# Kernel optimization log

Measured on AMD Instinct MI355X. Metric: run time of the kernel, lower is better.

Reference implementation:

```python
import jax, jax.numpy as jnp
import numpy as np

N_NODES = 100000
N_EDGES = 1600000
D_IN = 64
HID = 64
N_GRAPHS = 64
NEG_SLOPE = 0.2


def _glorot(k, shape):
    s = (6.0 / (shape[-2] + shape[-1])) ** 0.5
    return jax.random.uniform(k, shape, jnp.float32, -s, s)


def setup_inputs() -> dict:
    key = jax.random.key(0)
    ks = jax.random.split(key, 12)
    x = jax.random.normal(ks[0], (N_NODES, D_IN), jnp.float32)
    edge_index = jax.random.randint(ks[1], (2, N_EDGES), 0, N_NODES, dtype=jnp.int32)
    edge_attr = jax.random.normal(ks[2], (N_EDGES,), jnp.float32)
    batch = jnp.sort(jax.random.randint(ks[3], (N_NODES,), 0, N_GRAPHS, dtype=jnp.int32))
    inp = {"x": x, "edge_index": edge_index, "edge_attr": edge_attr, "batch": batch}
    dims = [(D_IN, HID), (HID, HID), (HID, HID)]
    for i, (din, dout) in enumerate(dims):
        inp[f"W{i}"] = _glorot(ks[4 + i], (din, dout))
        # att param is [1, heads=1, 2*out + nb_edge_feats=1] -> flatten to [2*out+1]
        inp[f"att{i}"] = _glorot(ks[7 + i], (1, 2 * dout + 1)).reshape(-1)
        inp[f"b{i}"] = jnp.zeros((dout,), jnp.float32)
    inp["Wf"] = _glorot(ks[10], (HID, 1))
    inp["bf"] = jnp.zeros((1,), jnp.float32)
    return inp


def _gat_layer(h, src, dst, e, valid, W, att, b, n):
    # MyGATConv (heads=1, concat=True): linear, per-edge attention logits,
    # leaky_relu, segment softmax over target nodes, weighted scatter-add.
    C = W.shape[1]
    h = h @ W                                  # [N, C]
    hi = h[dst]                                # gather target features per edge
    hj = h[src]                                # gather source features per edge
    logits = hi @ att[:C] + hj @ att[C:2 * C] + e * att[2 * C]  # [E]
    logits = jnp.where(logits >= 0, logits, NEG_SLOPE * logits)  # leaky_relu
    logits = jnp.where(valid, logits, -jnp.inf)  # drop original self-loops
    m = jax.ops.segment_max(logits, dst, num_segments=n)
    a = jnp.exp(logits - m[dst])
    a = jnp.where(valid, a, 0.0)
    denom = jax.ops.segment_sum(a, dst, num_segments=n)
    a = a / denom[dst]                         # segment softmax (self-loop guarantees denom>0)
    out = jax.ops.segment_sum(hj * a[:, None], dst, num_segments=n)
    return out + b


def reference(x, edge_index, edge_attr, batch, W0, att0, b0, W1, att1, b1, W2, att2, b2, Wf, bf):
    n = x.shape[0]
    src0, dst0 = edge_index[0], edge_index[1]
    loop = jnp.arange(n, dtype=src0.dtype)
    # remove_self_loops (via mask) + add_self_loops with edge_attr fill 0.0
    src = jnp.concatenate([src0, loop])
    dst = jnp.concatenate([dst0, loop])
    e = jnp.concatenate([edge_attr, jnp.zeros((n,), edge_attr.dtype)])
    valid = jnp.concatenate([src0 != dst0, jnp.ones((n,), bool)])
    h = x
    for (W, att, b) in ((W0, att0, b0), (W1, att1, b1), (W2, att2, b2)):
        h = jax.nn.relu(_gat_layer(h, src, dst, e, valid, W, att, b, n))
    pooled = jax.ops.segment_sum(h, batch, num_segments=N_GRAPHS)  # global_add_pool
    return (pooled @ Wf + bf).squeeze(-1)      # [N_GRAPHS]
```

## Files before the change

kernel.cpp:

```cpp
#include <hip/hip_runtime.h>
#include <math.h>

#define NNODES 100000
#define NEDGES 1600000
#define DIM 64
#define NGRAPHS 64
#define NEG_SLOPE 0.2f
#define SCAN_B 512
#define SCAN_NB ((NNODES + SCAN_B - 1) / SCAN_B)
#define MM_NB (NNODES / 16)
#define SCATTER_NB ((NEDGES / 4 + 255) / 256)


__global__ void zero_kernel(int* __restrict__ counts, float* __restrict__ pooled) {
    int i = blockIdx.x * blockDim.x + threadIdx.x;
    if (i <= NNODES) counts[i] = 0;
    if (i < NGRAPHS * DIM) pooled[i] = 0.f;
}

__global__ void hist_kernel(const int4* __restrict__ src4, const int4* __restrict__ dst4,
                            int* __restrict__ counts, int4* __restrict__ rank4) {
    int e = blockIdx.x * blockDim.x + threadIdx.x;
    if (e < NEDGES / 4) {
        int4 s = src4[e], d = dst4[e];
        int4 r;
        r.x = (s.x != d.x) ? atomicAdd(&counts[d.x], 1) : 0;
        r.y = (s.y != d.y) ? atomicAdd(&counts[d.y], 1) : 0;
        r.z = (s.z != d.z) ? atomicAdd(&counts[d.z], 1) : 0;
        r.w = (s.w != d.w) ? atomicAdd(&counts[d.w], 1) : 0;
        rank4[e] = r;
    }
}

__global__ void scan1_kernel(int* __restrict__ data, int* __restrict__ bsum) {
    __shared__ int tmp[SCAN_B];
    int t = threadIdx.x;
    int i = blockIdx.x * SCAN_B + t;
    int v = (i < NNODES) ? data[i] : 0;
    tmp[t] = v;
    __syncthreads();
    for (int off = 1; off < SCAN_B; off <<= 1) {
        int a = (t >= off) ? tmp[t - off] : 0;
        __syncthreads();
        if (t >= off) tmp[t] += a;
        __syncthreads();
    }
    if (i < NNODES) data[i] = tmp[t] - v;
    if (t == SCAN_B - 1) bsum[blockIdx.x] = tmp[t];
}

__global__ void scan2_kernel(int* __restrict__ bsum, int* __restrict__ total) {
    __shared__ int tmp[256];
    int t = threadIdx.x;
    int v = (t < SCAN_NB) ? bsum[t] : 0;
    tmp[t] = v;
    __syncthreads();
    for (int off = 1; off < 256; off <<= 1) {
        int a = (t >= off) ? tmp[t - off] : 0;
        __syncthreads();
        if (t >= off) tmp[t] += a;
        __syncthreads();
    }
    if (t < SCAN_NB) bsum[t] = tmp[t] - v;
    if (t == 255) *total = tmp[t];
}

__global__ void scan3_kernel(int* __restrict__ offs, const int* __restrict__ bsum,
                             const int* __restrict__ total) {
    int i = blockIdx.x * SCAN_B + threadIdx.x;
    if (i < NNODES) offs[i] = offs[i] + bsum[blockIdx.x];
    if (i == 0) offs[NNODES] = *total;
}

__global__ __launch_bounds__(256) void scatter_mm_kernel(
        const int4* __restrict__ src4, const int4* __restrict__ dst4,
        const float4* __restrict__ eattr4, const int4* __restrict__ rank4,
        const int* __restrict__ offs, int2* __restrict__ csr,
        const float* __restrict__ hin, const float* __restrict__ W,
        const float* __restrict__ att,
        float* __restrict__ h2, float* __restrict__ ad, float* __restrict__ as_) {
    __shared__ float wl[DIM * DIM];
    __shared__ float hrow[4 * 4 * DIM];
    if (blockIdx.x >= MM_NB) {
        int e = (blockIdx.x - MM_NB) * 256 + threadIdx.x;
        if (e < NEDGES / 4) {
            int4 s = src4[e], d = dst4[e];
            int4 r = rank4[e];
            float4 v = eattr4[e];
            if (s.x != d.x) csr[offs[d.x] + r.x] = make_int2(s.x, __float_as_int(v.x));
            if (s.y != d.y) csr[offs[d.y] + r.y] = make_int2(s.y, __float_as_int(v.y));
            if (s.z != d.z) csr[offs[d.z] + r.z] = make_int2(s.z, __float_as_int(v.z));
            if (s.w != d.w) csr[offs[d.w] + r.w] = make_int2(s.w, __float_as_int(v.w));
        }
        return;
    }
    int t = threadIdx.x;
    for (int k = t; k < DIM * DIM; k += 256) wl[k] = W[k];
    __syncthreads();
    int lane = t & 63, w = t >> 6;
    float a0 = att[lane], a1 = att[DIM + lane];
    int rbase = blockIdx.x * 16 + w * 4;
    float* hw = &hrow[w * 4 * DIM];
    #pragma unroll
    for (int r = 0; r < 4; ++r)
        hw[r * DIM + lane] = hin[(size_t)(rbase + r) * DIM + lane];
    float acc0 = 0.f, acc1 = 0.f, acc2 = 0.f, acc3 = 0.f;
    #pragma unroll
    for (int k = 0; k < DIM; ++k) {
        float wlk = wl[k * DIM + lane];
        acc0 = fmaf(hw[0 * DIM + k], wlk, acc0);
        acc1 = fmaf(hw[1 * DIM + k], wlk, acc1);
        acc2 = fmaf(hw[2 * DIM + k], wlk, acc2);
        acc3 = fmaf(hw[3 * DIM + k], wlk, acc3);
    }
    float accs[4] = {acc0, acc1, acc2, acc3};
    #pragma unroll
    for (int r = 0; r < 4; ++r) {
        int i = rbase + r;
        float acc = accs[r];
        h2[(size_t)i * DIM + lane] = acc;
        float vd = acc * a0, vs = acc * a1;
        #pragma unroll
        for (int off = 32; off; off >>= 1) {
            vd += __shfl_xor(vd, off, 64);
            vs += __shfl_xor(vs, off, 64);
        }
        if (lane == 0) { ad[i] = vd; as_[i] = vs; }
    }
}

__global__ __launch_bounds__(256) void mm_alpha_kernel(
        const float* __restrict__ hin, const float* __restrict__ W, const float* __restrict__ att,
        float* __restrict__ h2, float* __restrict__ ad, float* __restrict__ as_) {
    __shared__ float wl[DIM * DIM];
    __shared__ float hrow[4 * 4 * DIM];
    int t = threadIdx.x;
    for (int k = t; k < DIM * DIM; k += 256) wl[k] = W[k];
    __syncthreads();
    int lane = t & 63, w = t >> 6;
    float a0 = att[lane], a1 = att[DIM + lane];
    int rbase = blockIdx.x * 16 + w * 4;
    float* hw = &hrow[w * 4 * DIM];
    #pragma unroll
    for (int r = 0; r < 4; ++r)
        hw[r * DIM + lane] = hin[(size_t)(rbase + r) * DIM + lane];
    float acc0 = 0.f, acc1 = 0.f, acc2 = 0.f, acc3 = 0.f;
    #pragma unroll
    for (int k = 0; k < DIM; ++k) {
        float wlk = wl[k * DIM + lane];
        acc0 = fmaf(hw[0 * DIM + k], wlk, acc0);
        acc1 = fmaf(hw[1 * DIM + k], wlk, acc1);
        acc2 = fmaf(hw[2 * DIM + k], wlk, acc2);
        acc3 = fmaf(hw[3 * DIM + k], wlk, acc3);
    }
    float accs[4] = {acc0, acc1, acc2, acc3};
    #pragma unroll
    for (int r = 0; r < 4; ++r) {
        int i = rbase + r;
        float acc = accs[r];
        h2[(size_t)i * DIM + lane] = acc;
        float vd = acc * a0, vs = acc * a1;
        #pragma unroll
        for (int off = 32; off; off >>= 1) {
            vd += __shfl_xor(vd, off, 64);
            vs += __shfl_xor(vs, off, 64);
        }
        if (lane == 0) { ad[i] = vd; as_[i] = vs; }
    }
}

__global__ __launch_bounds__(256) void gat_agg_kernel(
        const float* __restrict__ h2, const float* __restrict__ ad, const float* __restrict__ as_,
        const int* __restrict__ offs, const int2* __restrict__ csr,
        const float* __restrict__ att, const float* __restrict__ bias, float* __restrict__ hout) {
    int t = threadIdx.x, lane = t & 63, w = t >> 6;
    int i = blockIdx.x * 4 + w;
    float att2 = att[2 * DIM];
    int beg = offs[i], end = offs[i + 1];
    float adi = ad[i];
    float ls = adi + as_[i];
    ls = ls >= 0.f ? ls : NEG_SLOPE * ls;
    float m = ls;
    float dsum = (lane == 0) ? 1.f : 0.f;
    float acc = h2[(size_t)i * DIM + lane];
    for (int e0 = beg; e0 < end; e0 += 64) {
        int e = e0 + lane;
        float l = -INFINITY;
        int s = 0;
        if (e < end) {
            int2 sv = csr[e];
            s = sv.x;
            l = adi + as_[s] + __int_as_float(sv.y) * att2;
            l = l >= 0.f ? l : NEG_SLOPE * l;
        }
        float bm = l;
        #pragma unroll
        for (int off = 32; off; off >>= 1) bm = fmaxf(bm, __shfl_xor(bm, off, 64));
        if (bm > m + 8.f) {
            float sc = __expf(m - bm);
            dsum *= sc; acc *= sc; m = bm;
        }
        float we = __expf(l - m);
        dsum += we;
        int cnt = min(64, end - e0);
        int j = 0;
        while (j + 8 <= cnt) {
            float v[8];
            #pragma unroll
            for (int k = 0; k < 8; ++k) {
                int sj = __shfl(s, j + k, 64);
                v[k] = h2[(size_t)sj * DIM + lane];
            }
            #pragma unroll
            for (int k = 0; k < 8; ++k) {
                float wgt = __shfl(we, j + k, 64);
                acc = fmaf(wgt, v[k], acc);
            }
            j += 8;
        }
        for (; j < cnt; ++j) {
            float wgt = __shfl(we, j, 64);
            int sj = __shfl(s, j, 64);
            acc = fmaf(wgt, h2[(size_t)sj * DIM + lane], acc);
        }
    }
    #pragma unroll
    for (int off = 32; off; off >>= 1) dsum += __shfl_xor(dsum, off, 64);
    float o = acc / dsum + bias[lane];
    hout[(size_t)i * DIM + lane] = fmaxf(o, 0.f);
}


__global__ __launch_bounds__(256) void pool_kernel(const float* __restrict__ h,
                                                   const int* __restrict__ batch,
                                                   float* __restrict__ pooled) {
    int t = threadIdx.x, lane = t & 63, w = t >> 6;
    int chunk = blockIdx.x * 4 + w;
    int i0 = chunk * 64;
    if (i0 >= NNODES) return;
    int iend = min(NNODES, i0 + 64);
    int cur = batch[i0];
    float acc = 0.f;
    for (int i = i0; i < iend; ++i) {
        int g = batch[i];
        if (g != cur) { atomicAdd(&pooled[cur * DIM + lane], acc); acc = 0.f; cur = g; }
        acc += h[(size_t)i * DIM + lane];
    }
    atomicAdd(&pooled[cur * DIM + lane], acc);
}

__global__ void final_kernel(const float* __restrict__ pooled, const float* __restrict__ Wf,
                             const float* __restrict__ bf, float* __restrict__ out) {
    int t = threadIdx.x, lane = t & 63, w = t >> 6;
    for (int g = w; g < NGRAPHS; g += 4) {
        float v = pooled[g * DIM + lane] * Wf[lane];
        #pragma unroll
        for (int off = 32; off; off >>= 1) v += __shfl_xor(v, off, 64);
        if (lane == 0) out[g] = v + bf[0];
    }
}


extern "C" void kernel_launch(void* const* d_in, const int* in_sizes, int n_in,
                              void* d_out, int out_size, void* d_ws, size_t ws_size,
                              hipStream_t stream) {
    const float* x      = (const float*)d_in[0];
    const int*   ei     = (const int*)d_in[1];
    const float* eattr  = (const float*)d_in[2];
    const int*   batch  = (const int*)d_in[3];
    const float* W[3]   = {(const float*)d_in[4], (const float*)d_in[7], (const float*)d_in[10]};
    const float* att[3] = {(const float*)d_in[5], (const float*)d_in[8], (const float*)d_in[11]};
    const float* bia[3] = {(const float*)d_in[6], (const float*)d_in[9], (const float*)d_in[12]};
    const float* Wf = (const float*)d_in[13];
    const float* bf = (const float*)d_in[14];
    float* out = (float*)d_out;
    const int* srcp = ei;
    const int* dstp = ei + NEDGES;

    char* p = (char*)d_ws;
    auto alloc = [&](size_t bytes) { char* r = p; p += (bytes + 255) & ~size_t(255); return r; };
    int*   offs    = (int*)alloc((NNODES + 1) * sizeof(int));
    int*   rank    = (int*)alloc((size_t)NEDGES * sizeof(int));
    int*   bsum    = (int*)alloc(SCAN_NB * sizeof(int));
    int*   total   = (int*)alloc(sizeof(int));
    int2*  csr     = (int2*)alloc((size_t)NEDGES * sizeof(int2));
    float* h2      = (float*)alloc((size_t)NNODES * DIM * sizeof(float));
    float* ad      = (float*)alloc(NNODES * sizeof(float));
    float* as_     = (float*)alloc(NNODES * sizeof(float));
    float* hbuf    = (float*)alloc((size_t)NNODES * DIM * sizeof(float));
    float* pooled  = (float*)alloc(NGRAPHS * DIM * sizeof(float));

    zero_kernel<<<(NNODES + 256) / 256, 256, 0, stream>>>(offs, pooled);
    hist_kernel<<<(NEDGES / 4 + 255) / 256, 256, 0, stream>>>(
        (const int4*)srcp, (const int4*)dstp, offs, (int4*)rank);
    scan1_kernel<<<SCAN_NB, SCAN_B, 0, stream>>>(offs, bsum);
    scan2_kernel<<<1, 256, 0, stream>>>(bsum, total);
    scan3_kernel<<<SCAN_NB, SCAN_B, 0, stream>>>(offs, bsum, total);

    scatter_mm_kernel<<<MM_NB + SCATTER_NB, 256, 0, stream>>>(
        (const int4*)srcp, (const int4*)dstp, (const float4*)eattr, (const int4*)rank,
        offs, csr, x, W[0], att[0], h2, ad, as_);
    gat_agg_kernel<<<NNODES / 4, 256, 0, stream>>>(h2, ad, as_, offs, csr,
                                                   att[0], bia[0], hbuf);

    for (int l = 1; l < 3; ++l) {
        mm_alpha_kernel<<<NNODES / 16, 256, 0, stream>>>(hbuf, W[l], att[l], h2, ad, as_);
        gat_agg_kernel<<<NNODES / 4, 256, 0, stream>>>(h2, ad, as_, offs, csr,
                                                       att[l], bia[l], hbuf);
    }

    pool_kernel<<<(((NNODES + 63) / 64) + 3) / 4, 256, 0, stream>>>(hbuf, batch, pooled);
    final_kernel<<<1, 256, 0, stream>>>(pooled, Wf, bf, out);
}
```

Before: 706.0 us.

## Fuse next-layer matmul and attention projections into GAT aggregation epilogue

Removes the separate mm_alpha kernel by having each aggregation block load the next layer's weight matrix into shared memory and compute the projected row plus attention dot products right after aggregating, with double-buffered h2/ad/as arrays. This avoids writing and re-reading the intermediate activation between layers. It also reorders the scatter/matmul block split so scatter blocks are scheduled first, and adds launch-bounds occupancy hints and a partial unroll. The cost is that every aggregation block now loads the 16KB weight matrix per 4 nodes, and uses extra LDS that may reduce occupancy.

```diff
diff --git a/kernel.cpp b/kernel.cpp
--- a/kernel.cpp
+++ b/kernel.cpp
@@ -72,7 +72,7 @@
     if (i == 0) offs[NNODES] = *total;
 }
 
-__global__ __launch_bounds__(256) void scatter_mm_kernel(
+__global__ __launch_bounds__(256, 4) void scatter_mm_kernel(
         const int4* __restrict__ src4, const int4* __restrict__ dst4,
         const float4* __restrict__ eattr4, const int4* __restrict__ rank4,
         const int* __restrict__ offs, int2* __restrict__ csr,
@@ -81,8 +81,8 @@
         float* __restrict__ h2, float* __restrict__ ad, float* __restrict__ as_) {
     __shared__ float wl[DIM * DIM];
     __shared__ float hrow[4 * 4 * DIM];
-    if (blockIdx.x >= MM_NB) {
-        int e = (blockIdx.x - MM_NB) * 256 + threadIdx.x;
+    if (blockIdx.x < SCATTER_NB) {
+        int e = blockIdx.x * 256 + threadIdx.x;
         if (e < NEDGES / 4) {
             int4 s = src4[e], d = dst4[e];
             int4 r = rank4[e];
@@ -94,18 +94,19 @@
         }
         return;
     }
+    int blk = blockIdx.x - SCATTER_NB;
     int t = threadIdx.x;
     for (int k = t; k < DIM * DIM; k += 256) wl[k] = W[k];
     __syncthreads();
     int lane = t & 63, w = t >> 6;
     float a0 = att[lane], a1 = att[DIM + lane];
-    int rbase = blockIdx.x * 16 + w * 4;
+    int rbase = blk * 16 + w * 4;
     float* hw = &hrow[w * 4 * DIM];
     #pragma unroll
     for (int r = 0; r < 4; ++r)
         hw[r * DIM + lane] = hin[(size_t)(rbase + r) * DIM + lane];
     float acc0 = 0.f, acc1 = 0.f, acc2 = 0.f, acc3 = 0.f;
-    #pragma unroll
+    #pragma unroll 16
     for (int k = 0; k < DIM; ++k) {
         float wlk = wl[k * DIM + lane];
         acc0 = fmaf(hw[0 * DIM + k], wlk, acc0);
@@ -129,51 +130,22 @@
     }
 }
 
-__global__ __launch_bounds__(256) void mm_alpha_kernel(
-        const float* __restrict__ hin, const float* __restrict__ W, const float* __restrict__ att,
-        float* __restrict__ h2, float* __restrict__ ad, float* __restrict__ as_) {
-    __shared__ float wl[DIM * DIM];
-    __shared__ float hrow[4 * 4 * DIM];
-    int t = threadIdx.x;
-    for (int k = t; k < DIM * DIM; k += 256) wl[k] = W[k];
-    __syncthreads();
-    int lane = t & 63, w = t >> 6;
-    float a0 = att[lane], a1 = att[DIM + lane];
-    int rbase = blockIdx.x * 16 + w * 4;
-    float* hw = &hrow[w * 4 * DIM];
-    #pragma unroll
-    for (int r = 0; r < 4; ++r)
-        hw[r * DIM + lane] = hin[(size_t)(rbase + r) * DIM + lane];
-    float acc0 = 0.f, acc1 = 0.f, acc2 = 0.f, acc3 = 0.f;
-    #pragma unroll
-    for (int k = 0; k < DIM; ++k) {
-        float wlk = wl[k * DIM + lane];
-        acc0 = fmaf(hw[0 * DIM + k], wlk, acc0);
-        acc1 = fmaf(hw[1 * DIM + k], wlk, acc1);
-        acc2 = fmaf(hw[2 * DIM + k], wlk, acc2);
-        acc3 = fmaf(hw[3 * DIM + k], wlk, acc3);
-    }
-    float accs[4] = {acc0, acc1, acc2, acc3};
-    #pragma unroll
-    for (int r = 0; r < 4; ++r) {
-        int i = rbase + r;
-        float acc = accs[r];
-        h2[(size_t)i * DIM + lane] = acc;
-        float vd = acc * a0, vs = acc * a1;
-        #pragma unroll
-        for (int off = 32; off; off >>= 1) {
-            vd += __shfl_xor(vd, off, 64);
-            vs += __shfl_xor(vs, off, 64);
-        }
-        if (lane == 0) { ad[i] = vd; as_[i] = vs; }
-    }
-}
-
 __global__ __launch_bounds__(256) void gat_agg_kernel(
         const float* __restrict__ h2, const float* __restrict__ ad, const float* __restrict__ as_,
         const int* __restrict__ offs, const int2* __restrict__ csr,
-        const float* __restrict__ att, const float* __restrict__ bias, float* __restrict__ hout) {
+        const float* __restrict__ att, const float* __restrict__ bias,
+        const float* __restrict__ Wnext, const float* __restrict__ attNext,
+        float* __restrict__ h2next, float* __restrict__ adNext, float* __restrict__ asNext,
+        float* __restrict__ hout) {
+    __shared__ float wl[DIM * DIM];
+    __shared__ float hrow[4 * DIM];
     int t = threadIdx.x, lane = t & 63, w = t >> 6;
+    if (Wnext) {
+        for (int k = t; k < DIM * DIM; k += 256) wl[k] = Wnext[k];
+        __syncthreads();
+    }
+    float a0n = 0.f, a1n = 0.f;
+    if (Wnext) { a0n = attNext[lane]; a1n = attNext[DIM + lane]; }
     int i = blockIdx.x * 4 + w;
     float att2 = att[2 * DIM];
     int beg = offs[i], end = offs[i + 1];
@@ -226,8 +198,24 @@
     }
     #pragma unroll
     for (int off = 32; off; off >>= 1) dsum += __shfl_xor(dsum, off, 64);
-    float o = acc / dsum + bias[lane];
-    hout[(size_t)i * DIM + lane] = fmaxf(o, 0.f);
+    float o = fmaxf(acc / dsum + bias[lane], 0.f);
+    if (!Wnext) {
+        hout[(size_t)i * DIM + lane] = o;
+        return;
+    }
+    hrow[w * DIM + lane] = o;
+    float h2v = 0.f;
+    #pragma unroll 8
+    for (int k = 0; k < DIM; ++k)
+        h2v = fmaf(hrow[w * DIM + k], wl[k * DIM + lane], h2v);
+    h2next[(size_t)i * DIM + lane] = h2v;
+    float vd = h2v * a0n, vs = h2v * a1n;
+    #pragma unroll
+    for (int off = 32; off; off >>= 1) {
+        vd += __shfl_xor(vd, off, 64);
+        vs += __shfl_xor(vs, off, 64);
+    }
+    if (lane == 0) { adNext[i] = vd; asNext[i] = vs; }
 }
 
 
@@ -284,10 +272,12 @@
     int*   bsum    = (int*)alloc(SCAN_NB * sizeof(int));
     int*   total   = (int*)alloc(sizeof(int));
     int2*  csr     = (int2*)alloc((size_t)NEDGES * sizeof(int2));
-    float* h2      = (float*)alloc((size_t)NNODES * DIM * sizeof(float));
-    float* ad      = (float*)alloc(NNODES * sizeof(float));
-    float* as_     = (float*)alloc(NNODES * sizeof(float));
-    float* hbuf    = (float*)alloc((size_t)NNODES * DIM * sizeof(float));
+    float* h2a     = (float*)alloc((size_t)NNODES * DIM * sizeof(float));
+    float* ad_a    = (float*)alloc(NNODES * sizeof(float));
+    float* as_a    = (float*)alloc(NNODES * sizeof(float));
+    float* h2b     = (float*)alloc((size_t)NNODES * DIM * sizeof(float));
+    float* ad_b    = (float*)alloc(NNODES * sizeof(float));
+    float* as_b    = (float*)alloc(NNODES * sizeof(float));
     float* pooled  = (float*)alloc(NGRAPHS * DIM * sizeof(float));
 
     zero_kernel<<<(NNODES + 256) / 256, 256, 0, stream>>>(offs, pooled);
@@ -297,18 +287,21 @@
     scan2_kernel<<<1, 256, 0, stream>>>(bsum, total);
     scan3_kernel<<<SCAN_NB, SCAN_B, 0, stream>>>(offs, bsum, total);
 
-    scatter_mm_kernel<<<MM_NB + SCATTER_NB, 256, 0, stream>>>(
+    scatter_mm_kernel<<<SCATTER_NB + MM_NB, 256, 0, stream>>>(
         (const int4*)srcp, (const int4*)dstp, (const float4*)eattr, (const int4*)rank,
-        offs, csr, x, W[0], att[0], h2, ad, as_);
-    gat_agg_kernel<<<NNODES / 4, 256, 0, stream>>>(h2, ad, as_, offs, csr,
-                                                   att[0], bia[0], hbuf);
-
-    for (int l = 1; l < 3; ++l) {
-        mm_alpha_kernel<<<NNODES / 16, 256, 0, stream>>>(hbuf, W[l], att[l], h2, ad, as_);
-        gat_agg_kernel<<<NNODES / 4, 256, 0, stream>>>(h2, ad, as_, offs, csr,
-                                                       att[l], bia[l], hbuf);
-    }
-
-    pool_kernel<<<(((NNODES + 63) / 64) + 3) / 4, 256, 0, stream>>>(hbuf, batch, pooled);
+        offs, csr, x, W[0], att[0], h2a, ad_a, as_a);
+
+    gat_agg_kernel<<<NNODES / 4, 256, 0, stream>>>(
+        h2a, ad_a, as_a, offs, csr, att[0], bia[0],
+        W[1], att[1], h2b, ad_b, as_b, (float*)nullptr);
+    gat_agg_kernel<<<NNODES / 4, 256, 0, stream>>>(
+        h2b, ad_b, as_b, offs, csr, att[1], bia[1],
+        W[2], att[2], h2a, ad_a, as_a, (float*)nullptr);
+    gat_agg_kernel<<<NNODES / 4, 256, 0, stream>>>(
+        h2a, ad_a, as_a, offs, csr, att[2], bia[2],
+        (const float*)nullptr, (const float*)nullptr,
+        (float*)nullptr, (float*)nullptr, (float*)nullptr, h2b);
+
+    pool_kernel<<<(((NNODES + 63) / 64) + 3) / 4, 256, 0, stream>>>(h2b, batch, pooled);
     final_kernel<<<1, 256, 0, stream>>>(pooled, Wf, bf, out);
 }
```

After: 596.2 us. 1.18x faster.
